# Kernel tuning notes

Measured on AMD Instinct MI355X. Metric: run time of the kernel, lower is better.

The kernel has to match this reference:

```python
import jax, jax.numpy as jnp
import numpy as np

B, F, D = 4096, 32, 32
LAYER_SIZE = [128, 128]


def setup_inputs() -> dict:
    key = jax.random.key(0)
    k1, k2, k3 = jax.random.split(key, 3)
    inputs = jax.random.normal(k1, (B, F, D), dtype=jnp.float32)
    # CIN filters: shape [1, field_nums[0]*field_nums[i], field_nums[i+1]]
    field_nums = [F] + LAYER_SIZE
    filter_0 = (jax.random.normal(k2, (1, field_nums[0] * field_nums[0], field_nums[1]), dtype=jnp.float32) * 0.05)
    filter_1 = (jax.random.normal(k3, (1, field_nums[0] * field_nums[1], field_nums[2]), dtype=jnp.float32) * 0.05)
    return {"inputs": inputs, "filter_0": filter_0, "filter_1": filter_1}


def _cin_forward(inputs, filters):
    x0 = inputs          # [B, F, D] -- hidden_nn_layers[0]
    prev = inputs        # hidden_nn_layers[-1]
    outs = []
    for W in filters:    # W: [1, F*M, N]
        # outer product over field dims: [B, F, M, D]
        z = jnp.einsum('bhd,bmd->bhmd', x0, prev)
        b, h, m, d = z.shape
        z = z.reshape(b, h * m, d)                 # [B, F*M, D]
        # 1x1 conv over the F*M axis == contraction with W[0]: [F*M, N]
        cur = jnp.einsum('bpd,pn->bnd', z, W[0])   # [B, N, D]
        cur = jax.nn.relu(cur)
        prev = cur
        outs.append(cur)
    result = jnp.concatenate(outs, axis=1)         # [B, sum(layer_size), D]
    return jnp.sum(result, axis=-1)                # [B, sum(layer_size)]


def reference(inputs, filter_0, filter_1):
    return _cin_forward(inputs, (filter_0, filter_1))
```

## Files before the change

### kernel.cpp

```cpp
#include <hip/hip_runtime.h>


typedef _Float16 half_t;
typedef _Float16 half4v __attribute__((ext_vector_type(4)));
typedef _Float16 half8 __attribute__((ext_vector_type(8)));
typedef float f32x16 __attribute__((ext_vector_type(16)));

__global__ void prep_w_kernel(const float* __restrict__ W0,
                              const float* __restrict__ W1,
                              half_t* __restrict__ Wp0,
                              half_t* __restrict__ Wp1) {
  int gid = blockIdx.x * 256 + threadIdx.x;
  int n = gid & 127;
  int tg = (gid >> 7) & 1;
  int s = gid >> 8;
  const float* W;
  half_t* Wp;
  int M, sl;
  if (s < 64) { W = W0; Wp = Wp0; M = 32; sl = s; }
  else        { W = W1; Wp = Wp1; M = 128; sl = s - 64; }
  int h = sl & 31, mc = sl >> 5;
  int kbase = h * M + mc * 16 + tg * 8;
  half8 v;
#pragma unroll
  for (int j = 0; j < 8; ++j) v[j] = (half_t)W[(size_t)(kbase + j) * 128 + n];
  *(half8*)(Wp + ((size_t)(sl * 2 + tg) * 128 + n) * 8) = v;
}

__device__ __forceinline__ int pswz(int row, int m) {
  return row * 128 + (((m >> 3) ^ (row & 15)) << 3) + (m & 7);
}

__device__ __forceinline__ f32x16 mfma3216(half8 a, half8 b, f32x16 c) {
  return __builtin_amdgcn_mfma_f32_32x32x16_f16(a, b, c, 0, 0, 0);
}

template <int MC, bool L1>
__device__ __forceinline__ void layer_loop(const half_t* __restrict__ Wp,
                                           const half_t* __restrict__ psrc,
                                           const half_t* __restrict__ xQb,
                                           int woff, int l31, int hi,
                                           f32x16 acc[2]) {
  half8 P[2];
#pragma unroll
  for (int bi = 0; bi < 2; ++bi)
    P[bi] = L1 ? *(const half8*)&psrc[(bi * 32 + l31) * 40 + hi * 8]
               : *(const half8*)&psrc[pswz(bi * 32 + l31, hi * 8)];

  half8 Br0 = *(const half8*)(Wp + (size_t)0 * 2048 + woff);
  half8 Br1 = *(const half8*)(Wp + (size_t)1 * 2048 + woff);
  half8 Br2 = *(const half8*)(Wp + (size_t)2 * 2048 + woff);
  half8 Br3 = *(const half8*)(Wp + (size_t)3 * 2048 + woff);

#pragma unroll 1
  for (int mc = 0; mc < MC; ++mc) {
#pragma unroll 1
    for (int p = 0; p < 8; ++p) {
      const int sb = mc * 32 + 4 * p;
      half8 xq = *(const half8*)(xQb + p * 256);

#define SSTEP(J, BR)                                                       \
  {                                                                        \
    half8 A0 = P[0] * xq[J * 2 + 0];                                       \
    half8 A1 = P[1] * xq[J * 2 + 1];                                       \
    acc[0] = mfma3216(A0, BR, acc[0]);                                     \
    acc[1] = mfma3216(A1, BR, acc[1]);                                     \
    BR = *(const half8*)(Wp +                                              \
                         (size_t)((sb + 4 + J) & (MC * 32 - 1)) * 2048 +   \
                         woff);                                            \
  }
      SSTEP(0, Br0)
      SSTEP(1, Br1)
      SSTEP(2, Br2)
      SSTEP(3, Br3)
#undef SSTEP
    }
    if (mc + 1 < MC) {
      const int mn = (mc + 1) * 16;
#pragma unroll
      for (int bi = 0; bi < 2; ++bi)
        P[bi] = L1 ? *(const half8*)&psrc[(bi * 32 + l31) * 40 + mn + hi * 8]
                   : *(const half8*)&psrc[pswz(bi * 32 + l31, mn + hi * 8)];
    }
  }
}

__global__ __launch_bounds__(256, 4) void cin_fused_kernel(
    const float* __restrict__ x0,
    const half_t* __restrict__ Wp0,
    const half_t* __restrict__ Wp1,
    float* __restrict__ out) {
  __shared__ half_t xQ[8 * 32 * 8];
  __shared__ half_t prevT[2 * 32 * 128];
  half_t* xT = prevT;

  const int tid = threadIdx.x;
  const int b0 = blockIdx.x * 2;

  const float4* x4 = (const float4*)(x0 + (size_t)b0 * 1024);
#pragma unroll
  for (int r = 0; r < 2; ++r) {
    int q = r * 256 + tid;
    float4 v = x4[q];
    int e4 = q * 4;
    int bi = e4 >> 10, h = (e4 >> 5) & 31, d0 = e4 & 31;
    half4v hv = {(half_t)v.x, (half_t)v.y, (half_t)v.z, (half_t)v.w};
#pragma unroll
    for (int j = 0; j < 4; ++j) {
      xQ[((h >> 2) * 32 + d0 + j) * 8 + (h & 3) * 2 + bi] = hv[j];
      xT[(bi * 32 + d0 + j) * 40 + h] = hv[j];
    }
  }
  __syncthreads();

  const int lane = tid & 63;
  const int l31 = lane & 31;
  const int hi = lane >> 5;
  const int wave = tid >> 6;

  const int woff = hi * 1024 + (wave * 32 + l31) * 8;
  const half_t* xQb = xQ + l31 * 8;

  f32x16 acc[2];
#pragma unroll
  for (int bi = 0; bi < 2; ++bi)
#pragma unroll
    for (int r = 0; r < 16; ++r) acc[bi][r] = 0.f;

  layer_loop<2, true>(Wp0, xT, xQb, woff, l31, hi, acc);

  __syncthreads();

#pragma unroll
  for (int bi = 0; bi < 2; ++bi) {
    float s = 0.f;
#pragma unroll
    for (int r = 0; r < 16; ++r) {
      float v = acc[bi][r];
      v = v > 0.f ? v : 0.f;
      s += v;
      int d = (r & 3) + ((r >> 2) << 3) + hi * 4;
      prevT[pswz(bi * 32 + d, wave * 32 + l31)] = (half_t)v;
      acc[bi][r] = 0.f;
    }
    s += __shfl_down(s, 32);
    if (lane < 32)
      out[(size_t)(b0 + bi) * 256 + wave * 32 + lane] = s;
  }
  __syncthreads();

  layer_loop<8, false>(Wp1, prevT, xQb, woff, l31, hi, acc);

#pragma unroll
  for (int bi = 0; bi < 2; ++bi) {
    float s = 0.f;
#pragma unroll
    for (int r = 0; r < 16; ++r) {
      float v = acc[bi][r];
      s += v > 0.f ? v : 0.f;
    }
    s += __shfl_down(s, 32);
    if (lane < 32)
      out[(size_t)(b0 + bi) * 256 + 128 + wave * 32 + lane] = s;
  }
}

extern "C" void kernel_launch(void* const* d_in, const int* in_sizes, int n_in,
                              void* d_out, int out_size, void* d_ws,
                              size_t ws_size, hipStream_t stream) {
  const float* x0 = (const float*)d_in[0];
  const float* w0 = (const float*)d_in[1];
  const float* w1 = (const float*)d_in[2];
  float* out = (float*)d_out;
  char* ws = (char*)d_ws;

  half_t* Wp0 = (half_t*)(ws);
  half_t* Wp1 = (half_t*)(ws + 64 * 2048 * 2);

  hipLaunchKernelGGL(prep_w_kernel, dim3(320), dim3(256), 0, stream, w0, w1,
                     Wp0, Wp1);
  hipLaunchKernelGGL(cin_fused_kernel, dim3(2048), dim3(256), 0, stream, x0,
                     Wp0, Wp1, out);
}
```

Baseline: 231.1 us.

## Use single-wave blocks computing 4 batches x 128 outputs for operand reuse

```diff
diff --git a/kernel.cpp b/kernel.cpp
--- a/kernel.cpp
+++ b/kernel.cpp
@@ -40,128 +40,156 @@
                                            const half_t* __restrict__ psrc,
                                            const half_t* __restrict__ xQb,
                                            int woff, int l31, int hi,
-                                           f32x16 acc[2]) {
-  half8 P[2];
-#pragma unroll
-  for (int bi = 0; bi < 2; ++bi)
+                                           f32x16 acc[4][4]) {
+  half8 P[4];
+#pragma unroll
+  for (int bi = 0; bi < 4; ++bi)
     P[bi] = L1 ? *(const half8*)&psrc[(bi * 32 + l31) * 40 + hi * 8]
                : *(const half8*)&psrc[pswz(bi * 32 + l31, hi * 8)];
 
-  half8 Br0 = *(const half8*)(Wp + (size_t)0 * 2048 + woff);
-  half8 Br1 = *(const half8*)(Wp + (size_t)1 * 2048 + woff);
-  half8 Br2 = *(const half8*)(Wp + (size_t)2 * 2048 + woff);
-  half8 Br3 = *(const half8*)(Wp + (size_t)3 * 2048 + woff);
+  half8 Br0[4], Br1[4];
+#pragma unroll
+  for (int j = 0; j < 4; ++j) {
+    Br0[j] = *(const half8*)(Wp + (size_t)0 * 2048 + woff + j * 256);
+    Br1[j] = *(const half8*)(Wp + (size_t)1 * 2048 + woff + j * 256);
+  }
+
+  half8 xq = *(const half8*)(xQb);
 
 #pragma unroll 1
   for (int mc = 0; mc < MC; ++mc) {
 #pragma unroll 1
-    for (int p = 0; p < 8; ++p) {
-      const int sb = mc * 32 + 4 * p;
-      half8 xq = *(const half8*)(xQb + p * 256);
-
-#define SSTEP(J, BR)                                                       \
-  {                                                                        \
-    half8 A0 = P[0] * xq[J * 2 + 0];                                       \
-    half8 A1 = P[1] * xq[J * 2 + 1];                                       \
-    acc[0] = mfma3216(A0, BR, acc[0]);                                     \
-    acc[1] = mfma3216(A1, BR, acc[1]);                                     \
-    BR = *(const half8*)(Wp +                                              \
-                         (size_t)((sb + 4 + J) & (MC * 32 - 1)) * 2048 +   \
-                         woff);                                            \
-  }
-      SSTEP(0, Br0)
-      SSTEP(1, Br1)
-      SSTEP(2, Br2)
-      SSTEP(3, Br3)
-#undef SSTEP
+    for (int hp = 0; hp < 16; ++hp) {
+      const int se = mc * 32 + 2 * hp;
+      half8 xqn = *(const half8*)(xQb + (((hp + 1) & 15) * 256));
+      {
+        half8 A0 = P[0] * xq[0], A1 = P[1] * xq[1], A2 = P[2] * xq[2],
+              A3 = P[3] * xq[3];
+#pragma unroll
+        for (int j = 0; j < 4; ++j) acc[0][j] = mfma3216(A0, Br0[j], acc[0][j]);
+#pragma unroll
+        for (int j = 0; j < 4; ++j) acc[1][j] = mfma3216(A1, Br0[j], acc[1][j]);
+#pragma unroll
+        for (int j = 0; j < 4; ++j) acc[2][j] = mfma3216(A2, Br0[j], acc[2][j]);
+#pragma unroll
+        for (int j = 0; j < 4; ++j) acc[3][j] = mfma3216(A3, Br0[j], acc[3][j]);
+        const half_t* Wps = Wp + (size_t)((se + 2) & (MC * 32 - 1)) * 2048;
+#pragma unroll
+        for (int j = 0; j < 4; ++j)
+          Br0[j] = *(const half8*)(Wps + woff + j * 256);
+      }
+      {
+        half8 A0 = P[0] * xq[4], A1 = P[1] * xq[5], A2 = P[2] * xq[6],
+              A3 = P[3] * xq[7];
+#pragma unroll
+        for (int j = 0; j < 4; ++j) acc[0][j] = mfma3216(A0, Br1[j], acc[0][j]);
+#pragma unroll
+        for (int j = 0; j < 4; ++j) acc[1][j] = mfma3216(A1, Br1[j], acc[1][j]);
+#pragma unroll
+        for (int j = 0; j < 4; ++j) acc[2][j] = mfma3216(A2, Br1[j], acc[2][j]);
+#pragma unroll
+        for (int j = 0; j < 4; ++j) acc[3][j] = mfma3216(A3, Br1[j], acc[3][j]);
+        const half_t* Wps = Wp + (size_t)((se + 3) & (MC * 32 - 1)) * 2048;
+#pragma unroll
+        for (int j = 0; j < 4; ++j)
+          Br1[j] = *(const half8*)(Wps + woff + j * 256);
+      }
+      xq = xqn;
     }
     if (mc + 1 < MC) {
       const int mn = (mc + 1) * 16;
 #pragma unroll
-      for (int bi = 0; bi < 2; ++bi)
+      for (int bi = 0; bi < 4; ++bi)
         P[bi] = L1 ? *(const half8*)&psrc[(bi * 32 + l31) * 40 + mn + hi * 8]
                    : *(const half8*)&psrc[pswz(bi * 32 + l31, mn + hi * 8)];
     }
   }
 }
 
-__global__ __launch_bounds__(256, 4) void cin_fused_kernel(
+__global__ __launch_bounds__(64, 1) void cin_fused_kernel(
     const float* __restrict__ x0,
     const half_t* __restrict__ Wp0,
     const half_t* __restrict__ Wp1,
     float* __restrict__ out) {
-  __shared__ half_t xQ[8 * 32 * 8];
-  __shared__ half_t prevT[2 * 32 * 128];
+  __shared__ half_t xQ[16 * 32 * 8];
+  __shared__ half_t prevT[4 * 32 * 128];
   half_t* xT = prevT;
 
   const int tid = threadIdx.x;
-  const int b0 = blockIdx.x * 2;
+  const int b0 = blockIdx.x * 4;
 
   const float4* x4 = (const float4*)(x0 + (size_t)b0 * 1024);
 #pragma unroll
-  for (int r = 0; r < 2; ++r) {
-    int q = r * 256 + tid;
+  for (int r = 0; r < 16; ++r) {
+    int q = r * 64 + tid;
     float4 v = x4[q];
     int e4 = q * 4;
     int bi = e4 >> 10, h = (e4 >> 5) & 31, d0 = e4 & 31;
     half4v hv = {(half_t)v.x, (half_t)v.y, (half_t)v.z, (half_t)v.w};
 #pragma unroll
     for (int j = 0; j < 4; ++j) {
-      xQ[((h >> 2) * 32 + d0 + j) * 8 + (h & 3) * 2 + bi] = hv[j];
+      xQ[((h >> 1) * 32 + d0 + j) * 8 + (h & 1) * 4 + bi] = hv[j];
       xT[(bi * 32 + d0 + j) * 40 + h] = hv[j];
     }
   }
   __syncthreads();
 
-  const int lane = tid & 63;
+  const int lane = tid;
   const int l31 = lane & 31;
   const int hi = lane >> 5;
-  const int wave = tid >> 6;
-
-  const int woff = hi * 1024 + (wave * 32 + l31) * 8;
+
+  const int woff = hi * 1024 + l31 * 8;
   const half_t* xQb = xQ + l31 * 8;
 
-  f32x16 acc[2];
-#pragma unroll
-  for (int bi = 0; bi < 2; ++bi)
-#pragma unroll
-    for (int r = 0; r < 16; ++r) acc[bi][r] = 0.f;
+  f32x16 acc[4][4];
+#pragma unroll
+  for (int bi = 0; bi < 4; ++bi)
+#pragma unroll
+    for (int j = 0; j < 4; ++j)
+#pragma unroll
+      for (int r = 0; r < 16; ++r) acc[bi][j][r] = 0.f;
 
   layer_loop<2, true>(Wp0, xT, xQb, woff, l31, hi, acc);
 
   __syncthreads();
 
 #pragma unroll
-  for (int bi = 0; bi < 2; ++bi) {
-    float s = 0.f;
-#pragma unroll
-    for (int r = 0; r < 16; ++r) {
-      float v = acc[bi][r];
-      v = v > 0.f ? v : 0.f;
-      s += v;
-      int d = (r & 3) + ((r >> 2) << 3) + hi * 4;
-      prevT[pswz(bi * 32 + d, wave * 32 + l31)] = (half_t)v;
-      acc[bi][r] = 0.f;
-    }
-    s += __shfl_down(s, 32);
-    if (lane < 32)
-      out[(size_t)(b0 + bi) * 256 + wave * 32 + lane] = s;
+  for (int bi = 0; bi < 4; ++bi) {
+#pragma unroll
+    for (int j = 0; j < 4; ++j) {
+      float s = 0.f;
+#pragma unroll
+      for (int r = 0; r < 16; ++r) {
+        float v = acc[bi][j][r];
+        v = v > 0.f ? v : 0.f;
+        s += v;
+        int d = (r & 3) + ((r >> 2) << 3) + hi * 4;
+        prevT[pswz(bi * 32 + d, j * 32 + l31)] = (half_t)v;
+        acc[bi][j][r] = 0.f;
+      }
+      s += __shfl_down(s, 32);
+      if (lane < 32)
+        out[(size_t)(b0 + bi) * 256 + j * 32 + lane] = s;
+    }
   }
   __syncthreads();
 
   layer_loop<8, false>(Wp1, prevT, xQb, woff, l31, hi, acc);
 
 #pragma unroll
-  for (int bi = 0; bi < 2; ++bi) {
-    float s = 0.f;
-#pragma unroll
-    for (int r = 0; r < 16; ++r) {
-      float v = acc[bi][r];
-      s += v > 0.f ? v : 0.f;
-    }
-    s += __shfl_down(s, 32);
-    if (lane < 32)
-      out[(size_t)(b0 + bi) * 256 + 128 + wave * 32 + lane] = s;
+  for (int bi = 0; bi < 4; ++bi) {
+#pragma unroll
+    for (int j = 0; j < 4; ++j) {
+      float s = 0.f;
+#pragma unroll
+      for (int r = 0; r < 16; ++r) {
+        float v = acc[bi][j][r];
+        s += v > 0.f ? v : 0.f;
+      }
+      s += __shfl_down(s, 32);
+      if (lane < 32)
+        out[(size_t)(b0 + bi) * 256 + 128 + j * 32 + lane] = s;
+    }
   }
 }
 
@@ -179,6 +207,6 @@
 
   hipLaunchKernelGGL(prep_w_kernel, dim3(320), dim3(256), 0, stream, w0, w1,
                      Wp0, Wp1);
-  hipLaunchKernelGGL(cin_fused_kernel, dim3(2048), dim3(256), 0, stream, x0,
+  hipLaunchKernelGGL(cin_fused_kernel, dim3(1024), dim3(64), 0, stream, x0,
                      Wp0, Wp1, out);
 }
```

Result: faster. 201.8 us (-12.7%).
